# Kernel optimization log

Measured on AMD Instinct MI355X. Metric: run time of the kernel, lower is better.

## Reference

```python
import jax, jax.numpy as jnp
import numpy as np

N = 50000
E = 800000
IN_DIM = 256
HID = 64
HEADS = 4
OUT_DIM = 40
NEG_SLOPE = 0.2


def _gatv2_conv(x, src, dst, Wl, bl, Wr, br, att, bias, concat):
    """PyG GATv2Conv (share_weights=False, eval mode, no attn dropout).
    src -> message source nodes, dst -> target nodes (softmax over dst)."""
    H, C = att.shape
    n = x.shape[0]
    xl = (x @ Wl + bl).reshape(n, H, C)  # source/message transform (lin_l)
    xr = (x @ Wr + br).reshape(n, H, C)  # target transform (lin_r)
    # per-edge logits: [E, H]
    s = xl[src] + xr[dst]                                  # [E,H,C]
    e = jnp.einsum('ehc,hc->eh', jax.nn.leaky_relu(s, NEG_SLOPE), att)
    # segment softmax over incoming edges of each target node
    m = jax.ops.segment_max(e, dst, num_segments=n)        # [N,H]
    m = jnp.where(jnp.isfinite(m), m, 0.0)                 # empty segments
    ex = jnp.exp(e - m[dst])
    denom = jax.ops.segment_sum(ex, dst, num_segments=n)   # [N,H]
    alpha = ex / (denom[dst] + 1e-16)                      # [E,H]
    out = jax.ops.segment_sum(alpha[:, :, None] * xl[src], dst, num_segments=n)
    if concat:
        out = out.reshape(n, H * C)
    else:
        out = out.mean(axis=1)
    return out + bias


def setup_inputs() -> dict:
    key = jax.random.key(0)
    ks = jax.random.split(key, 12)
    sc = 0.05
    return {
        'x': jax.random.normal(ks[0], (N, IN_DIM), jnp.float32),
        'src': jax.random.randint(ks[1], (E,), 0, N, jnp.int32),
        'dst': jax.random.randint(ks[2], (E,), 0, N, jnp.int32),
        'Wl1': jax.random.normal(ks[3], (IN_DIM, HEADS * HID), jnp.float32) * sc,
        'bl1': jnp.zeros((HEADS * HID,), jnp.float32),
        'Wr1': jax.random.normal(ks[4], (IN_DIM, HEADS * HID), jnp.float32) * sc,
        'br1': jnp.zeros((HEADS * HID,), jnp.float32),
        'att1': jax.random.normal(ks[5], (HEADS, HID), jnp.float32) * sc,
        'bias1': jnp.zeros((HEADS * HID,), jnp.float32),
        'Wl2': jax.random.normal(ks[6], (HEADS * HID, HEADS * HID), jnp.float32) * sc,
        'bl2': jnp.zeros((HEADS * HID,), jnp.float32),
        'Wr2': jax.random.normal(ks[7], (HEADS * HID, HEADS * HID), jnp.float32) * sc,
        'br2': jnp.zeros((HEADS * HID,), jnp.float32),
        'att2': jax.random.normal(ks[8], (HEADS, HID), jnp.float32) * sc,
        'bias2': jnp.zeros((HID,), jnp.float32),
        'Wc': jax.random.normal(ks[9], (HID, OUT_DIM), jnp.float32) * sc,
        'bc': jnp.zeros((OUT_DIM,), jnp.float32),
    }


def reference(x, src, dst, Wl1, bl1, Wr1, br1, att1, bias1,
              Wl2, bl2, Wr2, br2, att2, bias2, Wc, bc):
    h = _gatv2_conv(x, src, dst, Wl1, bl1, Wr1, br1, att1, bias1, concat=True)
    h = jax.nn.relu(h)  # dropout p applied only in training; eval -> identity
    h = _gatv2_conv(h, src, dst, Wl2, bl2, Wr2, br2, att2, bias2, concat=False)
    h = jax.nn.relu(h)
    return h @ Wc + bc  # [N, OUT_DIM]
```

## Files before the change

kernel.cpp:

```cpp
#include <hip/hip_runtime.h>
#include <hip/hip_bf16.h>
#include <math.h>


#define IN_DIM 256
#define HIDHC 256
#define HID 64
#define OUT_DIM 40

using half8  = __attribute__((ext_vector_type(8))) _Float16;
using half4  = __attribute__((ext_vector_type(4))) _Float16;
using half2v = __attribute__((ext_vector_type(2))) _Float16;
using f32x4  = __attribute__((ext_vector_type(4))) float;

__device__ __forceinline__ void gload16(const void* g, void* l) {
    __builtin_amdgcn_global_load_lds(
        (const __attribute__((address_space(1))) void*)g,
        (__attribute__((address_space(3))) void*)l, 16, 0, 0);
}


__global__ void edge_hist(const int* __restrict__ dst, int* __restrict__ deg, int E) {
    int i = blockIdx.x * blockDim.x + threadIdx.x;
    if (i < E) atomicAdd(&deg[dst[i]], 1);
}

__global__ void deg_block_reduce(const int* __restrict__ deg, int* __restrict__ bsum, int n) {
    int i = blockIdx.x * 256 + threadIdx.x;
    int v = (i < n) ? deg[i] : 0;
    #pragma unroll
    for (int off = 32; off; off >>= 1) v += __shfl_xor(v, off, 64);
    __shared__ int ws[4];
    int lane = threadIdx.x & 63, wid = threadIdx.x >> 6;
    if (lane == 0) ws[wid] = v;
    __syncthreads();
    if (threadIdx.x == 0) bsum[blockIdx.x] = ws[0] + ws[1] + ws[2] + ws[3];
}

__global__ void scan_bsums(const int* __restrict__ bsum, int* __restrict__ bpre, int nb) {
    __shared__ int s[256];
    int tid = threadIdx.x;
    int orig = (tid < nb) ? bsum[tid] : 0;
    s[tid] = orig;
    __syncthreads();
    #pragma unroll
    for (int off = 1; off < 256; off <<= 1) {
        int t = (tid >= off) ? s[tid - off] : 0;
        __syncthreads();
        s[tid] += t;
        __syncthreads();
    }
    if (tid < nb) bpre[tid] = s[tid] - orig;
}

__global__ void deg_scan_apply(const int* __restrict__ deg, const int* __restrict__ bpre,
                               int* __restrict__ offsets, int* __restrict__ cursor, int n) {
    int i = blockIdx.x * 256 + threadIdx.x;
    int lane = threadIdx.x & 63, wid = threadIdx.x >> 6;
    int v = (i < n) ? deg[i] : 0;
    int inc = v;
    #pragma unroll
    for (int off = 1; off < 64; off <<= 1) {
        int t = __shfl_up(inc, off, 64);
        if (lane >= off) inc += t;
    }
    __shared__ int ws[4];
    if (lane == 63) ws[wid] = inc;
    __syncthreads();
    int add = bpre[blockIdx.x];
    for (int w = 0; w < wid; ++w) add += ws[w];
    int incl = inc + add;
    if (i < n) { offsets[i + 1] = incl; cursor[i] = incl - v; }
    if (i == 0) offsets[0] = 0;
}

__global__ void edge_scatter(const int* __restrict__ src, const int* __restrict__ dst,
                             int* __restrict__ cursor, int* __restrict__ csr_src, int E) {
    int i = blockIdx.x * blockDim.x + threadIdx.x;
    if (i < E) {
        int p = atomicAdd(&cursor[dst[i]], 1);
        csr_src[p] = src[i];
    }
}


__global__ void cvt_f16_tiled(const float* __restrict__ in, _Float16* __restrict__ out, int n4) {
    int i = blockIdx.x * blockDim.x + threadIdx.x;
    if (i >= n4) return;
    float4 v = ((const float4*)in)[i];
    half4 h = { (_Float16)v.x, (_Float16)v.y, (_Float16)v.z, (_Float16)v.w };
    int node = i >> 6;
    int kb = (i & 63) * 4;
    size_t a = (size_t)(node >> 7) * 32768 + (size_t)(kb >> 3) * 1024
             + (size_t)(node & 127) * 8 + (kb & 7);
    *(half4*)(out + a) = h;
}

__global__ void prep_weights(const float* __restrict__ W0, const float* __restrict__ W1,
                             const float* __restrict__ W2, const float* __restrict__ W3,
                             _Float16* __restrict__ T) {
    const float* Wsel = (blockIdx.y == 0) ? W0 : (blockIdx.y == 1) ? W1
                      : (blockIdx.y == 2) ? W2 : W3;
    int k = blockIdx.x, nn = threadIdx.x;
    float v = Wsel[k * 256 + nn];
    size_t a = (size_t)blockIdx.y * 65536
             + (size_t)(nn >> 7) * 32768 + (size_t)(k >> 5) * 4096
             + (size_t)((k >> 3) & 3) * 1024 + (size_t)(nn & 127) * 8 + (k & 7);
    T[a] = (_Float16)v;
}


__global__ __launch_bounds__(512) void gemm_dual(
    const _Float16* __restrict__ Apk,
    const _Float16* __restrict__ W0, const float* __restrict__ b0, _Float16* __restrict__ C0,
    const _Float16* __restrict__ W1, const float* __restrict__ b1, _Float16* __restrict__ C1,
    int M)
{
    __shared__ __align__(16) _Float16 sA[2][4096];
    __shared__ __align__(16) _Float16 sW[2][2][4096];

    int tid = threadIdx.x;
    int bm = blockIdx.x * 128;
    int bn = blockIdx.y * 128;

    int lane = tid & 63, w = tid >> 6;
    int z  = w >> 2, wq = w & 3;
    int r = lane & 15, q = lane >> 4;
    int m0 = (wq >> 1) * 64, n0 = (wq & 1) * 64;

    const _Float16* Abase = Apk + (size_t)blockIdx.x * 32768;
    const _Float16* W0b   = W0  + (size_t)blockIdx.y * 32768;
    const _Float16* W1b   = W1  + (size_t)blockIdx.y * 32768;
    int go = tid * 8;

    f32x4 acc[4][4];
    #pragma unroll
    for (int i = 0; i < 4; ++i)
        #pragma unroll
        for (int j = 0; j < 4; ++j) acc[i][j] = (f32x4)0.f;

    gload16(Abase + go, &sA[0][go]);
    gload16(W0b + go, &sW[0][0][go]);
    gload16(W1b + go, &sW[0][1][go]);
    __builtin_amdgcn_s_waitcnt(0);
    __syncthreads();

    #pragma unroll 1
    for (int kt = 0; kt < 8; ++kt) {
        int buf = kt & 1;
        if (kt < 7) {
            int k0 = (kt + 1) * 4096;
            gload16(Abase + k0 + go, &sA[buf ^ 1][go]);
            gload16(W0b + k0 + go, &sW[buf ^ 1][0][go]);
            gload16(W1b + k0 + go, &sW[buf ^ 1][1][go]);
        }
        half8 a[4], b[4];
        #pragma unroll
        for (int i = 0; i < 4; ++i) {
            a[i] = *(const half8*)(&sA[buf][(q * 128 + m0 + i * 16 + r) * 8]);
            b[i] = *(const half8*)(&sW[buf][z][(q * 128 + n0 + i * 16 + r) * 8]);
        }
        #pragma unroll
        for (int i = 0; i < 4; ++i)
            #pragma unroll
            for (int j = 0; j < 4; ++j)
                acc[i][j] = __builtin_amdgcn_mfma_f32_16x16x32_f16(a[i], b[j], acc[i][j], 0, 0, 0);
        __builtin_amdgcn_s_waitcnt(0);
        __syncthreads();
    }

    const float* bias = z ? b1 : b0;
    _Float16*    C    = z ? C1 : C0;

    float bv[4];
    #pragma unroll
    for (int j = 0; j < 4; ++j) bv[j] = bias[bn + n0 + j * 16 + r];
    #pragma unroll
    for (int i = 0; i < 4; ++i) {
        #pragma unroll
        for (int reg = 0; reg < 4; ++reg) {
            int orow = bm + m0 + i * 16 + q * 4 + reg;
            if (orow < M) {
                #pragma unroll
                for (int j = 0; j < 4; ++j)
                    C[(size_t)orow * 256 + bn + n0 + j * 16 + r] =
                        (_Float16)(acc[i][j][reg] + bv[j]);
            }
        }
    }
}


__global__ __launch_bounds__(256) void gat_node(
    const _Float16* __restrict__ xl, const _Float16* __restrict__ xr,
    const float* __restrict__ att, const float* __restrict__ bias,
    const int* __restrict__ offsets, const int* __restrict__ csr_src,
    void* __restrict__ out0, int n, int mode)
{
    int wid = threadIdx.x >> 6;
    int node = (blockIdx.x << 2) + wid;
    if (node >= n) return;
    int lane = threadIdx.x & 63;
    int H = lane >> 5;
    int p = lane & 31;

    const half2v c02 = { (_Float16)0.2f, (_Float16)0.2f };

    half8 xrh = *(const half8*)(xr + (size_t)node * HIDHC + p * 8);
    half2v xr01 = __builtin_shufflevector(xrh, xrh, 0, 1);
    half2v xr23 = __builtin_shufflevector(xrh, xrh, 2, 3);
    half2v xr45 = __builtin_shufflevector(xrh, xrh, 4, 5);
    half2v xr67 = __builtin_shufflevector(xrh, xrh, 6, 7);

    float4 af0 = *(const float4*)(att + p * 8);
    float4 af1 = *(const float4*)(att + p * 8 + 4);
    half2v at01 = { (_Float16)af0.x, (_Float16)af0.y };
    half2v at23 = { (_Float16)af0.z, (_Float16)af0.w };
    half2v at45 = { (_Float16)af1.x, (_Float16)af1.y };
    half2v at67 = { (_Float16)af1.z, (_Float16)af1.w };

    float acc[8];
    #pragma unroll
    for (int k = 0; k < 8; ++k) acc[k] = 0.f;
    float d = 0.f;

    auto edge_compute = [&](half8 h) {
        half2v h01 = __builtin_shufflevector(h, h, 0, 1);
        half2v h23 = __builtin_shufflevector(h, h, 2, 3);
        half2v h45 = __builtin_shufflevector(h, h, 4, 5);
        half2v h67 = __builtin_shufflevector(h, h, 6, 7);
        half2v s01 = h01 + xr01, s23 = h23 + xr23, s45 = h45 + xr45, s67 = h67 + xr67;
        half2v l01 = __builtin_elementwise_max(s01, s01 * c02);
        half2v l23 = __builtin_elementwise_max(s23, s23 * c02);
        half2v l45 = __builtin_elementwise_max(s45, s45 * c02);
        half2v l67 = __builtin_elementwise_max(s67, s67 * c02);
        float e = __builtin_amdgcn_fdot2(l01, at01, 0.f, false);
        e = __builtin_amdgcn_fdot2(l23, at23, e, false);
        e = __builtin_amdgcn_fdot2(l45, at45, e, false);
        e = __builtin_amdgcn_fdot2(l67, at67, e, false);
        e += __shfl_xor(e, 1);
        e += __shfl_xor(e, 2);
        e += __shfl_xor(e, 4);
        float pw = __expf(e);
        d += pw;
        #pragma unroll
        for (int k = 0; k < 8; ++k) acc[k] = fmaf(pw, (float)h[k], acc[k]);
    };

    int j0 = __builtin_amdgcn_readfirstlane(offsets[node]);
    int j1 = __builtin_amdgcn_readfirstlane(offsets[node + 1]);
    int deg = j1 - j0;

    int fast = min(deg, 64);
    int npf = fast >> 1;
    int idxv = 0;
    if (lane < fast) idxv = csr_src[j0 + lane];

    half8 hA, hB;
    if (npf > 0) { int s = __shfl(idxv, 0 + H, 64); hA = *(const half8*)(xl + (size_t)s * HIDHC + p * 8); }
    if (npf > 1) { int s = __shfl(idxv, 2 + H, 64); hB = *(const half8*)(xl + (size_t)s * HIDHC + p * 8); }
    int t = 0;
    for (; t + 4 <= npf; t += 2) {
        half8 ha = hA, hb = hB;
        { int s = __shfl(idxv, (t + 2) * 2 + H, 64); hA = *(const half8*)(xl + (size_t)s * HIDHC + p * 8); }
        { int s = __shfl(idxv, (t + 3) * 2 + H, 64); hB = *(const half8*)(xl + (size_t)s * HIDHC + p * 8); }
        edge_compute(ha);
        edge_compute(hb);
    }
    if (t + 2 <= npf) {
        half8 ha = hA, hb = hB;
        if (t + 2 < npf) { int s = __shfl(idxv, (t + 2) * 2 + H, 64); hA = *(const half8*)(xl + (size_t)s * HIDHC + p * 8); }
        edge_compute(ha);
        edge_compute(hb);
        t += 2;
    }
    if (t < npf) {
        edge_compute(hA);
    }

    int j = j0 + (npf << 1);
    for (; j + 2 <= j1; j += 2) {
        int s0 = __builtin_amdgcn_readfirstlane(csr_src[j]);
        int s1 = __builtin_amdgcn_readfirstlane(csr_src[j + 1]);
        int s = H ? s1 : s0;
        half8 h = *(const half8*)(xl + (size_t)s * HIDHC + p * 8);
        edge_compute(h);
    }
    if (j < j1) {
        int s0 = __builtin_amdgcn_readfirstlane(csr_src[j]);
        half8 h = *(const half8*)(xl + (size_t)s0 * HIDHC + p * 8);
        half2v h01 = __builtin_shufflevector(h, h, 0, 1);
        half2v h23 = __builtin_shufflevector(h, h, 2, 3);
        half2v h45 = __builtin_shufflevector(h, h, 4, 5);
        half2v h67 = __builtin_shufflevector(h, h, 6, 7);
        half2v s01 = h01 + xr01, s23 = h23 + xr23, s45 = h45 + xr45, s67 = h67 + xr67;
        half2v l01 = __builtin_elementwise_max(s01, s01 * c02);
        half2v l23 = __builtin_elementwise_max(s23, s23 * c02);
        half2v l45 = __builtin_elementwise_max(s45, s45 * c02);
        half2v l67 = __builtin_elementwise_max(s67, s67 * c02);
        float e = __builtin_amdgcn_fdot2(l01, at01, 0.f, false);
        e = __builtin_amdgcn_fdot2(l23, at23, e, false);
        e = __builtin_amdgcn_fdot2(l45, at45, e, false);
        e = __builtin_amdgcn_fdot2(l67, at67, e, false);
        e += __shfl_xor(e, 1);
        e += __shfl_xor(e, 2);
        e += __shfl_xor(e, 4);
        float pw = (H == 0) ? __expf(e) : 0.f;
        d += pw;
        #pragma unroll
        for (int k = 0; k < 8; ++k) acc[k] = fmaf(pw, (float)h[k], acc[k]);
    }

    d += __shfl_xor(d, 32);
    #pragma unroll
    for (int k = 0; k < 8; ++k) acc[k] += __shfl_xor(acc[k], 32);

    float inv = 1.f / (d + 1e-16f);
    float o[8];
    #pragma unroll
    for (int k = 0; k < 8; ++k) o[k] = acc[k] * inv;

    if (mode == 0) {
        if (H == 0) {
            float4 b0 = *(const float4*)(bias + p * 8);
            float4 b1 = *(const float4*)(bias + p * 8 + 4);
            float bb[8] = { b0.x, b0.y, b0.z, b0.w, b1.x, b1.y, b1.z, b1.w };
            half8 hh;
            #pragma unroll
            for (int k = 0; k < 8; ++k) hh[k] = (_Float16)fmaxf(o[k] + bb[k], 0.f);
            _Float16* dst = (_Float16*)out0 + (size_t)(node >> 7) * 32768
                          + (size_t)p * 1024 + (size_t)(node & 127) * 8;
            *(half8*)dst = hh;
        }
    } else {
        #pragma unroll
        for (int k = 0; k < 8; ++k) {
            o[k] += __shfl_xor(o[k], 8);
            o[k] += __shfl_xor(o[k], 16);
        }
        if (lane < 8) {
            float4 b0 = *(const float4*)(bias + p * 8);
            float4 b1 = *(const float4*)(bias + p * 8 + 4);
            float bb[8] = { b0.x, b0.y, b0.z, b0.w, b1.x, b1.y, b1.z, b1.w };
            float4 o0, o1;
            o0.x = fmaxf(o[0] * 0.25f + bb[0], 0.f);
            o0.y = fmaxf(o[1] * 0.25f + bb[1], 0.f);
            o0.z = fmaxf(o[2] * 0.25f + bb[2], 0.f);
            o0.w = fmaxf(o[3] * 0.25f + bb[3], 0.f);
            o1.x = fmaxf(o[4] * 0.25f + bb[4], 0.f);
            o1.y = fmaxf(o[5] * 0.25f + bb[5], 0.f);
            o1.z = fmaxf(o[6] * 0.25f + bb[6], 0.f);
            o1.w = fmaxf(o[7] * 0.25f + bb[7], 0.f);
            float* dst = (float*)out0 + (size_t)node * HID + p * 8;
            *(float4*)dst = o0;
            *(float4*)(dst + 4) = o1;
        }
    }
}


__global__ __launch_bounds__(256) void final_linear(
    const float* __restrict__ h2, const float* __restrict__ Wc,
    const float* __restrict__ bc, float* __restrict__ out, int n)
{
    __shared__ float Ws[HID * OUT_DIM];
    __shared__ float bs[OUT_DIM];
    __shared__ float hs[64][HID + 1];

    for (int i = threadIdx.x; i < HID * OUT_DIM; i += 256) Ws[i] = Wc[i];
    if (threadIdx.x < OUT_DIM) bs[threadIdx.x] = bc[threadIdx.x];

    int n0 = blockIdx.x * 64;
    for (int i = threadIdx.x; i < 64 * HID; i += 256) {
        int r = i >> 6, c = i & 63;
        int node = n0 + r;
        hs[r][c] = (node < n) ? h2[(size_t)node * HID + c] : 0.f;
    }
    __syncthreads();

    for (int idx = threadIdx.x; idx < 64 * OUT_DIM; idx += 256) {
        int r = idx / OUT_DIM, o = idx % OUT_DIM;
        int node = n0 + r;
        if (node < n) {
            float s = bs[o];
            #pragma unroll
            for (int c = 0; c < HID; ++c) s = fmaf(hs[r][c], Ws[c * OUT_DIM + o], s);
            out[(size_t)node * OUT_DIM + o] = s;
        }
    }
}


extern "C" void kernel_launch(void* const* d_in, const int* in_sizes, int n_in,
                              void* d_out, int out_size, void* d_ws, size_t ws_size,
                              hipStream_t stream) {
    const int N = in_sizes[0] / IN_DIM;
    const int E = in_sizes[1];

    const float* x    = (const float*)d_in[0];
    const int*   src  = (const int*)d_in[1];
    const int*   dst  = (const int*)d_in[2];
    const float* Wl1  = (const float*)d_in[3];
    const float* bl1  = (const float*)d_in[4];
    const float* Wr1  = (const float*)d_in[5];
    const float* br1  = (const float*)d_in[6];
    const float* att1 = (const float*)d_in[7];
    const float* bias1= (const float*)d_in[8];
    const float* Wl2  = (const float*)d_in[9];
    const float* bl2  = (const float*)d_in[10];
    const float* Wr2  = (const float*)d_in[11];
    const float* br2  = (const float*)d_in[12];
    const float* att2 = (const float*)d_in[13];
    const float* bias2= (const float*)d_in[14];
    const float* Wc   = (const float*)d_in[15];
    const float* bc   = (const float*)d_in[16];

    char* ws = (char*)d_ws;
    size_t off = 0;
    const int NT = (N + 127) / 128;
    _Float16* xlh = (_Float16*)(ws + off); off += (size_t)N * HIDHC * 2;
    _Float16* xrh = (_Float16*)(ws + off); off += (size_t)N * HIDHC * 2;
    _Float16* Af  = (_Float16*)(ws + off); off += (size_t)NT * 32768 * 2;
    float*    h2  = (float*)(ws + off);    off += (size_t)N * HID * 4;
    _Float16* Wt  = (_Float16*)(ws + off); off += (size_t)4 * 65536 * 2;
    int* deg     = (int*)(ws + off); off += (size_t)N * 4;
    int* offsets = (int*)(ws + off); off += (size_t)(N + 1) * 4;
    int* cursor  = (int*)(ws + off); off += (size_t)N * 4;
    int* csr     = (int*)(ws + off); off += (size_t)E * 4;
    int* bsum    = (int*)(ws + off); off += 256 * 4;
    int* bpre    = (int*)(ws + off); off += 256 * 4;

    const int NB = (N + 255) / 256;

    hipMemsetAsync(deg, 0, (size_t)N * 4, stream);
    if (N & 127)
        hipMemsetAsync(Af + (size_t)(NT - 1) * 32768, 0, 32768 * 2, stream);
    edge_hist<<<(E + 255) / 256, 256, 0, stream>>>(dst, deg, E);
    deg_block_reduce<<<NB, 256, 0, stream>>>(deg, bsum, N);
    scan_bsums<<<1, 256, 0, stream>>>(bsum, bpre, NB);
    deg_scan_apply<<<NB, 256, 0, stream>>>(deg, bpre, offsets, cursor, N);
    edge_scatter<<<(E + 255) / 256, 256, 0, stream>>>(src, dst, cursor, csr, E);
    prep_weights<<<dim3(256, 4), 256, 0, stream>>>(Wl1, Wr1, Wl2, Wr2, Wt);
    cvt_f16_tiled<<<(N * HIDHC / 4 + 255) / 256, 256, 0, stream>>>(x, Af, N * HIDHC / 4);

    const int KW = 65536;
    dim3 gg(NT, 2);
    gemm_dual<<<gg, 512, 0, stream>>>(Af,
        Wt + 0 * KW, bl1, xlh,
        Wt + 1 * KW, br1, xrh, N);
    gat_node<<<(N + 3) / 4, 256, 0, stream>>>(xlh, xrh, att1, bias1, offsets, csr,
                                              (void*)Af, N, 0);
    gemm_dual<<<gg, 512, 0, stream>>>(Af,
        Wt + 2 * KW, bl2, xlh,
        Wt + 3 * KW, br2, xrh, N);
    gat_node<<<(N + 3) / 4, 256, 0, stream>>>(xlh, xrh, att2, bias2, offsets, csr,
                                              (void*)h2, N, 1);
    final_linear<<<(N + 63) / 64, 256, 0, stream>>>(h2, Wc, bc, (float*)d_out, N);
}
```

Before: 428.0 us.

## Triple-buffer LDS tiles in dual GEMM with two-deep prefetch and partial waits

Changes the dual projection GEMM from double to triple buffering in LDS. Two k-tiles are now in flight, and each iteration waits only for the oldest one (vmcnt(3)) instead of draining every outstanding load, so global loads overlap more with MFMA work. The loop is fully unrolled to make buffer indices compile-time constants. LDS per block grows from 48KB to 72KB, which may cut occupancy. Dropping the LDS wait before the barrier relies on the vmcnt semantics of global_load_lds being correct.

```diff
diff --git a/kernel.cpp b/kernel.cpp
--- a/kernel.cpp
+++ b/kernel.cpp
@@ -116,8 +116,8 @@
     const _Float16* __restrict__ W1, const float* __restrict__ b1, _Float16* __restrict__ C1,
     int M)
 {
-    __shared__ __align__(16) _Float16 sA[2][4096];
-    __shared__ __align__(16) _Float16 sW[2][2][4096];
+    __shared__ __align__(16) _Float16 sA[3][4096];
+    __shared__ __align__(16) _Float16 sW[3][2][4096];
 
     int tid = threadIdx.x;
     int bm = blockIdx.x * 128;
@@ -139,20 +139,25 @@
         #pragma unroll
         for (int j = 0; j < 4; ++j) acc[i][j] = (f32x4)0.f;
 
-    gload16(Abase + go, &sA[0][go]);
-    gload16(W0b + go, &sW[0][0][go]);
-    gload16(W1b + go, &sW[0][1][go]);
-    __builtin_amdgcn_s_waitcnt(0);
-    __syncthreads();
-
-    #pragma unroll 1
+    gload16(Abase + 0 * 4096 + go, &sA[0][go]);
+    gload16(W0b   + 0 * 4096 + go, &sW[0][0][go]);
+    gload16(W1b   + 0 * 4096 + go, &sW[0][1][go]);
+    gload16(Abase + 1 * 4096 + go, &sA[1][go]);
+    gload16(W0b   + 1 * 4096 + go, &sW[1][0][go]);
+    gload16(W1b   + 1 * 4096 + go, &sW[1][1][go]);
+    asm volatile("s_waitcnt vmcnt(3)" ::: "memory");
+    __builtin_amdgcn_s_barrier();
+    __builtin_amdgcn_sched_barrier(0);
+
+    #pragma unroll
     for (int kt = 0; kt < 8; ++kt) {
-        int buf = kt & 1;
-        if (kt < 7) {
-            int k0 = (kt + 1) * 4096;
-            gload16(Abase + k0 + go, &sA[buf ^ 1][go]);
-            gload16(W0b + k0 + go, &sW[buf ^ 1][0][go]);
-            gload16(W1b + k0 + go, &sW[buf ^ 1][1][go]);
+        const int buf = kt % 3;
+        if (kt < 6) {
+            const int nb = (kt + 2) % 3;
+            const int k0 = (kt + 2) * 4096;
+            gload16(Abase + k0 + go, &sA[nb][go]);
+            gload16(W0b   + k0 + go, &sW[nb][0][go]);
+            gload16(W1b   + k0 + go, &sW[nb][1][go]);
         }
         half8 a[4], b[4];
         #pragma unroll
@@ -165,8 +170,15 @@
             #pragma unroll
             for (int j = 0; j < 4; ++j)
                 acc[i][j] = __builtin_amdgcn_mfma_f32_16x16x32_f16(a[i], b[j], acc[i][j], 0, 0, 0);
-        __builtin_amdgcn_s_waitcnt(0);
-        __syncthreads();
+        if (kt < 6) {
+            asm volatile("s_waitcnt vmcnt(3)" ::: "memory");
+        } else if (kt == 6) {
+            asm volatile("s_waitcnt vmcnt(0)" ::: "memory");
+        }
+        if (kt < 7) {
+            __builtin_amdgcn_s_barrier();
+            __builtin_amdgcn_sched_barrier(0);
+        }
     }
 
     const float* bias = z ? b1 : b0;
```

After: 441.4 us. +3.1%, slower.
